# Performance work log

Hardware: AMD Instinct MI355X
Metric: run time of the kernel (lower is better)

Reference implementation:

```python
import jax, jax.numpy as jnp
import numpy as np

CH = 128
MID = CH // 4  # 32
B, H, W = 16, 128, 128


def _phi(x):
    # elu(x) + 1 (alpha=1)
    return jax.nn.elu(x) + 1.0


def setup_inputs() -> dict:
    key = jax.random.key(0)
    ks = jax.random.split(key, 6)
    x = jax.random.normal(ks[0], (B, CH, H, W), dtype=jnp.float32)
    Wq = jax.random.normal(ks[1], (MID, CH), dtype=jnp.float32) * 0.05
    Wk = jax.random.normal(ks[2], (MID, CH), dtype=jnp.float32) * 0.05
    Wv = jax.random.normal(ks[3], (MID, CH), dtype=jnp.float32) * 0.05
    Wout = jax.random.normal(ks[4], (CH, MID), dtype=jnp.float32) * 0.05
    gamma = jnp.ones((CH,), dtype=jnp.float32)
    beta = jnp.zeros((CH,), dtype=jnp.float32)
    return {"x": x, "Wq": Wq, "Wk": Wk, "Wv": Wv, "Wout": Wout,
            "gamma": gamma, "beta": beta}


def reference(x, Wq, Wk, Wv, Wout, gamma, beta):
    b, c, h, w = x.shape
    n = h * w
    xf = x.reshape(b, c, n)                      # [B, C, N]
    # 1x1 convs == channel matmuls
    Q = _phi(jnp.einsum('mc,bcn->bmn', Wq, xf))  # [B, M, N]
    K = _phi(jnp.einsum('mc,bcn->bmn', Wk, xf))  # [B, M, N]
    V = jnp.einsum('mc,bcn->bmn', Wv, xf)        # [B, M, N]
    # KV-first linear attention
    KV = jnp.einsum('bmn,bvn->bmv', K, V)        # [B, M, M]
    out = jnp.einsum('bmv,bvn->bmn', KV, Q) / (n + 1e-6)  # [B, M, N]
    Ks = jnp.sum(K, axis=-1, keepdims=True)      # [B, M, 1]
    denom = jnp.sum(Q * Ks, axis=1, keepdims=True) + 1e-6  # [B, 1, N]
    out = out / denom
    # output 1x1 conv
    y = jnp.einsum('cm,bmn->bcn', Wout, out).reshape(b, c, h, w)
    # BatchNorm2d (training-mode forward: batch statistics, biased var, eps=1e-5)
    mean = jnp.mean(y, axis=(0, 2, 3), keepdims=True)
    var = jnp.var(y, axis=(0, 2, 3), keepdims=True)
    y = (y - mean) * jax.lax.rsqrt(var + 1e-5)
    y = y * gamma[None, :, None, None] + beta[None, :, None, None]
    return y
```

## Files before the change

### kernel.cpp

```cpp
#include <hip/hip_runtime.h>

#define BB 16
#define CC 128
#define MM 32
#define NN 16384

#define WS_KV     0
#define WS_KS     16384
#define WS_SQ     16896
#define WS_QQ     17408
#define WS_YSUM   33792
#define WS_YSQ    33920
#define WS_ACCEND 34048
#define WS_W2     34304

typedef __bf16 bf16x8 __attribute__((ext_vector_type(8)));
typedef __bf16 bf16x4 __attribute__((ext_vector_type(4)));
typedef float  f32x16 __attribute__((ext_vector_type(16)));

union B8 { bf16x8 v8; bf16x4 v4[2]; };

__device__ __forceinline__ float phi_f(float z) {
    return z > 0.f ? z + 1.f : __expf(z);
}

__device__ __forceinline__ void lds_barrier() {
    asm volatile("s_waitcnt lgkmcnt(0)" ::: "memory");
    __builtin_amdgcn_sched_barrier(0);
    __builtin_amdgcn_s_barrier();
    __builtin_amdgcn_sched_barrier(0);
}

__global__ void zero_kernel(float* ws) {
    const int i = blockIdx.x * 256 + threadIdx.x;
    if (i < (WS_ACCEND / 4)) {
        float4 z; z.x = 0.f; z.y = 0.f; z.z = 0.f; z.w = 0.f;
        ((float4*)ws)[i] = z;
    }
}

__global__ __launch_bounds__(256) void projmfma_kernel(
    const float* __restrict__ x,
    const float* __restrict__ Wq, const float* __restrict__ Wk,
    const float* __restrict__ Wv,
    float* ws, float* __restrict__ qout)
{
    __shared__ __align__(16) char smem[71680];
    __bf16* Xh  = (__bf16*)smem;
    __bf16* ktH = (__bf16*)(smem + 34816);
    __bf16* ktL = (__bf16*)(smem + 44032);
    __bf16* vtH = (__bf16*)(smem + 53248);
    __bf16* vtL = (__bf16*)(smem + 62464);

    const int b = blockIdx.y;
    const int t = threadIdx.x;
    const int w = t >> 6;
    const int l = t & 63;
    const int g = l >> 5;
    const int ln31 = l & 31;

    bf16x8 wh[8], wl[8];
    if (w < 3) {
        const float* Wm = (w == 0) ? Wq : (w == 1) ? Wk : Wv;
        const float* wr = Wm + ln31 * CC;
        #pragma unroll
        for (int kt = 0; kt < 8; ++kt) {
            const int k0 = 16 * kt + 8 * g;
            #pragma unroll
            for (int j = 0; j < 8; ++j) {
                const float f = wr[k0 + j];
                const __bf16 h = (__bf16)f;
                wh[kt][j] = h;
                wl[kt][j] = (__bf16)(f - (float)h);
            }
        }
    }

    f32x16 kvA, ksA;
    bf16x8 ones;
    #pragma unroll
    for (int i = 0; i < 16; ++i) { kvA[i] = 0.f; ksA[i] = 0.f; }
    #pragma unroll
    for (int j = 0; j < 8; ++j) ones[j] = (__bf16)1.0f;

    const int px = t & 63;
    const int cb = t >> 6;

    const float* xbase = x + (size_t)b * CC * NN + (blockIdx.x << 9) + px;

    for (int tile = 0; tile < 8; ++tile) {
        const int cur = tile & 1;
        const int n0 = (blockIdx.x << 9) + (tile << 6);

        {
            const float* xp = xbase + (tile << 6);
            float xb[32];
            #pragma unroll
            for (int j = 0; j < 32; ++j)
                xb[j] = xp[(size_t)(cb * 32 + j) * NN];
            __bf16 hb[32];
            #pragma unroll
            for (int j = 0; j < 32; ++j) hb[j] = (__bf16)xb[j];
            #pragma unroll
            for (int q = 0; q < 4; ++q)
                *(bf16x8*)&Xh[cur * 8704 + px * 136 + cb * 32 + q * 8] =
                    *(bf16x8*)&hb[q * 8];
        }
        lds_barrier();

        if (w < 3) {
            f32x16 a0, a1;
            #pragma unroll
            for (int i = 0; i < 16; ++i) { a0[i] = 0.f; a1[i] = 0.f; }
            const __bf16* xh = Xh + cur * 8704;
            #pragma unroll
            for (int kt = 0; kt < 8; ++kt) {
                const int k0 = 16 * kt + 8 * g;
                const bf16x8 b0 = *(const bf16x8*)&xh[ln31 * 136 + k0];
                const bf16x8 b1 = *(const bf16x8*)&xh[(ln31 + 32) * 136 + k0];
                a0 = __builtin_amdgcn_mfma_f32_32x32x16_bf16(wh[kt], b0, a0, 0, 0, 0);
                a0 = __builtin_amdgcn_mfma_f32_32x32x16_bf16(wl[kt], b0, a0, 0, 0, 0);
                a1 = __builtin_amdgcn_mfma_f32_32x32x16_bf16(wh[kt], b1, a1, 0, 0, 0);
                a1 = __builtin_amdgcn_mfma_f32_32x32x16_bf16(wl[kt], b1, a1, 0, 0, 0);
            }
            if (w == 0) {
                float* qp = qout + (size_t)b * CC * NN + n0 + ln31;
                #pragma unroll
                for (int i = 0; i < 16; ++i) {
                    const int r = (i & 3) + 8 * (i >> 2) + 4 * g;
                    qp[(size_t)r * NN]      = phi_f(a0[i]);
                    qp[(size_t)r * NN + 32] = phi_f(a1[i]);
                }
            } else if (w == 1) {
                __bf16* kh = ktH + cur * 2304;
                __bf16* kl = ktL + cur * 2304;
                #pragma unroll
                for (int i = 0; i < 16; ++i) {
                    const int r = (i & 3) + 8 * (i >> 2) + 4 * g;
                    const float f0 = phi_f(a0[i]);
                    const float f1 = phi_f(a1[i]);
                    const __bf16 h0 = (__bf16)f0;
                    const __bf16 h1 = (__bf16)f1;
                    kh[r * 72 + ln31]      = h0;
                    kl[r * 72 + ln31]      = (__bf16)(f0 - (float)h0);
                    kh[r * 72 + 32 + ln31] = h1;
                    kl[r * 72 + 32 + ln31] = (__bf16)(f1 - (float)h1);
                }
            } else {
                __bf16* vh = vtH + cur * 2304;
                __bf16* vl = vtL + cur * 2304;
                #pragma unroll
                for (int i = 0; i < 16; ++i) {
                    const int r = (i & 3) + 8 * (i >> 2) + 4 * g;
                    const float f0 = a0[i];
                    const float f1 = a1[i];
                    const __bf16 h0 = (__bf16)f0;
                    const __bf16 h1 = (__bf16)f1;
                    vh[r * 72 + ln31]      = h0;
                    vl[r * 72 + ln31]      = (__bf16)(f0 - (float)h0);
                    vh[r * 72 + 32 + ln31] = h1;
                    vl[r * 72 + 32 + ln31] = (__bf16)(f1 - (float)h1);
                }
            }
        } else if (tile > 0) {
            const int pb = (cur ^ 1) * 2304;
            const __bf16* khp = ktH + pb + ln31 * 72;
            const __bf16* klp = ktL + pb + ln31 * 72;
            const __bf16* vhp = vtH + pb + ln31 * 72;
            const __bf16* vlp = vtL + pb + ln31 * 72;
            #pragma unroll
            for (int s = 0; s < 4; ++s) {
                const int k0 = s * 16 + g * 8;
                const bf16x8 akh = *(const bf16x8*)&khp[k0];
                const bf16x8 akl = *(const bf16x8*)&klp[k0];
                const bf16x8 bvh = *(const bf16x8*)&vhp[k0];
                const bf16x8 bvl = *(const bf16x8*)&vlp[k0];
                kvA = __builtin_amdgcn_mfma_f32_32x32x16_bf16(akh, bvh, kvA, 0, 0, 0);
                kvA = __builtin_amdgcn_mfma_f32_32x32x16_bf16(akh, bvl, kvA, 0, 0, 0);
                kvA = __builtin_amdgcn_mfma_f32_32x32x16_bf16(akl, bvh, kvA, 0, 0, 0);
                ksA = __builtin_amdgcn_mfma_f32_32x32x16_bf16(akh, ones, ksA, 0, 0, 0);
                ksA = __builtin_amdgcn_mfma_f32_32x32x16_bf16(akl, ones, ksA, 0, 0, 0);
            }
        }
        lds_barrier();
    }

    if (w == 3) {
        const int pb = 2304;
        const __bf16* khp = ktH + pb + ln31 * 72;
        const __bf16* klp = ktL + pb + ln31 * 72;
        const __bf16* vhp = vtH + pb + ln31 * 72;
        const __bf16* vlp = vtL + pb + ln31 * 72;
        #pragma unroll
        for (int s = 0; s < 4; ++s) {
            const int k0 = s * 16 + g * 8;
            const bf16x8 akh = *(const bf16x8*)&khp[k0];
            const bf16x8 akl = *(const bf16x8*)&klp[k0];
            const bf16x8 bvh = *(const bf16x8*)&vhp[k0];
            const bf16x8 bvl = *(const bf16x8*)&vlp[k0];
            kvA = __builtin_amdgcn_mfma_f32_32x32x16_bf16(akh, bvh, kvA, 0, 0, 0);
            kvA = __builtin_amdgcn_mfma_f32_32x32x16_bf16(akh, bvl, kvA, 0, 0, 0);
            kvA = __builtin_amdgcn_mfma_f32_32x32x16_bf16(akl, bvh, kvA, 0, 0, 0);
            ksA = __builtin_amdgcn_mfma_f32_32x32x16_bf16(akh, ones, ksA, 0, 0, 0);
            ksA = __builtin_amdgcn_mfma_f32_32x32x16_bf16(akl, ones, ksA, 0, 0, 0);
        }
        float* kvb = ws + WS_KV + (b << 10);
        #pragma unroll
        for (int i = 0; i < 16; ++i) {
            const int r = (i & 3) + 8 * (i >> 2) + 4 * g;
            atomicAdd(&kvb[r * 32 + ln31], kvA[i]);
        }
        if (ln31 == 0) {
            #pragma unroll
            for (int i = 0; i < 16; ++i) {
                const int r = (i & 3) + 8 * (i >> 2) + 4 * g;
                atomicAdd(&ws[WS_KS + (b << 5) + r], ksA[i]);
            }
        }
    }
}

__global__ __launch_bounds__(256) void qq_kernel(const float* qsrc, float* ws) {
    __shared__ __align__(16) char qsm[33792];
    __bf16* Qh = (__bf16*)qsm;
    __bf16* Ql = (__bf16*)(qsm + 16896);
    float*  red   = (float*)qsm;
    float*  sqred = (float*)(qsm + 17408);

    const int b = blockIdx.y;
    const int t = threadIdx.x;
    const int w = t >> 6;
    const int l = t & 63;
    const int g = l >> 5;
    const int ln31 = l & 31;

    const float* ksb = ws + WS_KS + (b << 5);
    const int n = (blockIdx.x << 8) + t;
    const float* qp = qsrc + (size_t)b * CC * NN + n;

    float qa[32];
    #pragma unroll
    for (int m = 0; m < 32; ++m) qa[m] = qp[(size_t)m * NN];

    float denom = 1e-6f;
    #pragma unroll
    for (int m = 0; m < 32; ++m) denom = fmaf(qa[m], ksb[m], denom);
    const float inv = 1.0f / (16384.0f * denom);
    #pragma unroll
    for (int m = 0; m < 32; ++m) qa[m] *= inv;

    #pragma unroll
    for (int m = 0; m < 32; ++m) {
        const __bf16 h = (__bf16)qa[m];
        Qh[m * 264 + t] = h;
        Ql[m * 264 + t] = (__bf16)(qa[m] - (float)h);
    }
    __syncthreads();

    f32x16 qqA, sqA;
    bf16x8 ones;
    #pragma unroll
    for (int i = 0; i < 16; ++i) { qqA[i] = 0.f; sqA[i] = 0.f; }
    #pragma unroll
    for (int j = 0; j < 8; ++j) ones[j] = (__bf16)1.0f;

    #pragma unroll
    for (int sub = 0; sub < 2; ++sub) {
        #pragma unroll
        for (int s = 0; s < 2; ++s) {
            const int k0 = (w << 6) + (sub << 5) + s * 16 + g * 8;
            const bf16x8 ah = *(const bf16x8*)&Qh[ln31 * 264 + k0];
            const bf16x8 al = *(const bf16x8*)&Ql[ln31 * 264 + k0];
            qqA = __builtin_amdgcn_mfma_f32_32x32x16_bf16(ah, ah, qqA, 0, 0, 0);
            qqA = __builtin_amdgcn_mfma_f32_32x32x16_bf16(ah, al, qqA, 0, 0, 0);
            qqA = __builtin_amdgcn_mfma_f32_32x32x16_bf16(al, ah, qqA, 0, 0, 0);
            sqA = __builtin_amdgcn_mfma_f32_32x32x16_bf16(ah, ones, sqA, 0, 0, 0);
            sqA = __builtin_amdgcn_mfma_f32_32x32x16_bf16(al, ones, sqA, 0, 0, 0);
        }
    }
    __syncthreads();

    #pragma unroll
    for (int i = 0; i < 16; ++i) red[t * 17 + i] = qqA[i];
    if (ln31 == 0) {
        #pragma unroll
        for (int i = 0; i < 16; ++i) {
            const int r = (i & 3) + 8 * (i >> 2) + 4 * g;
            sqred[(w << 5) + r] = sqA[i];
        }
    }
    __syncthreads();
    if (t < 64) {
        float* qqb = ws + WS_QQ + (b << 10);
        #pragma unroll
        for (int i = 0; i < 16; ++i) {
            const int r = (i & 3) + 8 * (i >> 2) + 4 * g;
            const float s = red[t*17+i] + red[(t+64)*17+i] + red[(t+128)*17+i] + red[(t+192)*17+i];
            atomicAdd(&qqb[r * 32 + ln31], s);
        }
    }
    if (t < 32) {
        const float s = sqred[t] + sqred[32 + t] + sqred[64 + t] + sqred[96 + t];
        atomicAdd(&ws[WS_SQ + (b << 5) + t], s);
    }
}

__global__ __launch_bounds__(128) void bnstat_kernel(const float* __restrict__ Wout,
                                                     float* ws) {
    const int b = blockIdx.x;
    const int c = threadIdx.x;
    const float* kvb = ws + WS_KV + (b << 10);
    const float* wo  = Wout + (c << 5);
    float w[32];
    #pragma unroll
    for (int v = 0; v < 32; ++v) w[v] = 0.f;
    for (int m = 0; m < 32; ++m) {
        const float wm = wo[m];
        #pragma unroll
        for (int v = 0; v < 32; ++v) w[v] = fmaf(wm, kvb[(m << 5) + v], w[v]);
    }
    float* w2b = ws + WS_W2 + (b << 12) + (c << 5);
    #pragma unroll
    for (int v = 0; v < 32; ++v) w2b[v] = w[v];

    const float* sq = ws + WS_SQ + (b << 5);
    const float* qq = ws + WS_QQ + (b << 10);
    float mb = 0.f;
    #pragma unroll
    for (int v = 0; v < 32; ++v) mb = fmaf(w[v], sq[v], mb);
    float qf = 0.f;
    for (int u = 0; u < 32; ++u) {
        float tacc = 0.f;
        #pragma unroll
        for (int v = 0; v < 32; ++v) tacc = fmaf(qq[(u << 5) + v], w[v], tacc);
        qf = fmaf(w[u], tacc, qf);
    }
    atomicAdd(&ws[WS_YSUM + c], mb);
    atomicAdd(&ws[WS_YSQ + c], qf);
}

__global__ __launch_bounds__(256) void out_kernel(const float* qsrc, const float* ws,
                                                  const float* __restrict__ gamma,
                                                  const float* __restrict__ beta,
                                                  float* out) {
    __shared__ __align__(16) __bf16 Qh[256 * 36];
    __shared__ __align__(16) __bf16 Ql[256 * 36];
    __shared__ float scs[CC];
    __shared__ float bis[CC];

    const int b = blockIdx.y;
    const int t = threadIdx.x;
    const int w = t >> 6;
    const int l = t & 63;
    const int g = l >> 5;
    const int ln31 = l & 31;

    if (t < CC) {
        const float invBN = 1.0f / 262144.0f;
        const float mean = ws[WS_YSUM + t] * invBN;
        const float var  = ws[WS_YSQ + t] * invBN - mean * mean;
        const float s = gamma[t] * rsqrtf(var + 1e-5f);
        scs[t] = s;
        bis[t] = fmaf(-mean, s, beta[t]);
    }

    const int n = (blockIdx.x << 8) + t;
    const float* ksb = ws + WS_KS + (b << 5);

    const float* qp = qsrc + (size_t)b * CC * NN + n;
    float qa[32];
    #pragma unroll
    for (int m = 0; m < 32; ++m) qa[m] = qp[(size_t)m * NN];

    float d0 = 1e-6f;
    #pragma unroll
    for (int m = 0; m < 32; ++m) d0 = fmaf(qa[m], ksb[m], d0);
    const float inv = 1.0f / (16384.0f * d0);
    #pragma unroll
    for (int m = 0; m < 32; ++m) qa[m] *= inv;

    {
        __bf16 qh[32], ql[32];
        #pragma unroll
        for (int m = 0; m < 32; ++m) {
            const __bf16 h = (__bf16)qa[m];
            qh[m] = h;
            ql[m] = (__bf16)(qa[m] - (float)h);
        }
        #pragma unroll
        for (int i = 0; i < 8; ++i) {
            *(bf16x4*)&Qh[t * 36 + i * 4] = *(bf16x4*)&qh[i * 4];
            *(bf16x4*)&Ql[t * 36 + i * 4] = *(bf16x4*)&ql[i * 4];
        }
    }
    __syncthreads();

    const float* w2b = ws + WS_W2 + (b << 12);
    float* ob = out + (size_t)b * CC * NN + (blockIdx.x << 8);

    #pragma unroll
    for (int cb = 0; cb < 4; ++cb) {
        bf16x8 ah[2], al[2];
        #pragma unroll
        for (int kt = 0; kt < 2; ++kt) {
            const float* wp = w2b + (cb * 32 + ln31) * 32 + kt * 16 + g * 8;
            #pragma unroll
            for (int j = 0; j < 8; ++j) {
                const float f = wp[j];
                const __bf16 h = (__bf16)f;
                ah[kt][j] = h;
                al[kt][j] = (__bf16)(f - (float)h);
            }
        }
        #pragma unroll
        for (int pg = 0; pg < 2; ++pg) {
            const int px0 = (w << 6) + (pg << 5);
            f32x16 acc;
            #pragma unroll
            for (int i = 0; i < 16; ++i) acc[i] = 0.f;
            #pragma unroll
            for (int kt = 0; kt < 2; ++kt) {
                const int k0 = kt * 16 + g * 8;
                const __bf16* qhp = &Qh[(px0 + ln31) * 36 + k0];
                const __bf16* qlp = &Ql[(px0 + ln31) * 36 + k0];
                B8 bh, bl;
                bh.v4[0] = *(const bf16x4*)&qhp[0];
                bh.v4[1] = *(const bf16x4*)&qhp[4];
                bl.v4[0] = *(const bf16x4*)&qlp[0];
                bl.v4[1] = *(const bf16x4*)&qlp[4];
                acc = __builtin_amdgcn_mfma_f32_32x32x16_bf16(ah[kt], bh.v8, acc, 0, 0, 0);
                acc = __builtin_amdgcn_mfma_f32_32x32x16_bf16(ah[kt], bl.v8, acc, 0, 0, 0);
                acc = __builtin_amdgcn_mfma_f32_32x32x16_bf16(al[kt], bh.v8, acc, 0, 0, 0);
            }
            #pragma unroll
            for (int i = 0; i < 16; ++i) {
                const int r = (i & 3) + 8 * (i >> 2) + 4 * g;
                const int c = cb * 32 + r;
                const float v = fmaf(scs[c], acc[i], bis[c]);
                __builtin_nontemporal_store(v, &ob[(size_t)c * NN + px0 + ln31]);
            }
        }
    }
}

extern "C" void kernel_launch(void* const* d_in, const int* in_sizes, int n_in,
                              void* d_out, int out_size, void* d_ws, size_t ws_size,
                              hipStream_t stream) {
    const float* x     = (const float*)d_in[0];
    const float* Wq    = (const float*)d_in[1];
    const float* Wk    = (const float*)d_in[2];
    const float* Wv    = (const float*)d_in[3];
    const float* Wout  = (const float*)d_in[4];
    const float* gamma = (const float*)d_in[5];
    const float* beta  = (const float*)d_in[6];
    float* ws  = (float*)d_ws;
    float* out = (float*)d_out;

    zero_kernel<<<34, 256, 0, stream>>>(ws);
    projmfma_kernel<<<dim3(32, 16), 256, 0, stream>>>(x, Wq, Wk, Wv, ws, out);
    qq_kernel<<<dim3(64, 16), 256, 0, stream>>>(out, ws);
    bnstat_kernel<<<16, 128, 0, stream>>>(Wout, ws);
    out_kernel<<<dim3(64, 16), 256, 0, stream>>>(out, ws, gamma, beta, out);
}
```

Baseline: 110.8 us.

## Split projection into one 64-pixel tile per block with prepacked bf16 weights

The projection kernel now handles one 64-pixel tile per block instead of looping over eight tiles, growing the grid from 512 to 4096 blocks. LDS is halved by dropping double buffering. A separate small kernel pre-splits the Q/K/V weights into hi/lo bf16 once, so each block loads packed weights instead of converting them. The KV accumulation is spread across all four waves and reduced in LDS before the global atomics. The aim is more occupancy and latency hiding. The cost is eight times more global atomics on KV/Ks, an extra kernel launch, and a weight reload per block.

```diff
diff --git a/kernel.cpp b/kernel.cpp
--- a/kernel.cpp
+++ b/kernel.cpp
@@ -13,6 +13,7 @@
 #define WS_YSQ    33920
 #define WS_ACCEND 34048
 #define WS_W2     34304
+#define WS_WPACK  99840
 
 typedef __bf16 bf16x8 __attribute__((ext_vector_type(8)));
 typedef __bf16 bf16x4 __attribute__((ext_vector_type(4)));
@@ -39,18 +40,33 @@
     }
 }
 
+__global__ void wpack_kernel(const float* __restrict__ Wq,
+                             const float* __restrict__ Wk,
+                             const float* __restrict__ Wv, float* ws) {
+    __bf16* wp = (__bf16*)(ws + WS_WPACK);
+    const int idx = blockIdx.x * 256 + threadIdx.x;
+    if (idx < 12288) {
+        const int mi  = idx >> 12;
+        const int rem = idx & 4095;
+        const float f = (mi == 0 ? Wq : mi == 1 ? Wk : Wv)[rem];
+        const __bf16 h = (__bf16)f;
+        wp[idx]         = h;
+        wp[12288 + idx] = (__bf16)(f - (float)h);
+    }
+}
+
 __global__ __launch_bounds__(256) void projmfma_kernel(
-    const float* __restrict__ x,
-    const float* __restrict__ Wq, const float* __restrict__ Wk,
-    const float* __restrict__ Wv,
+    const float* __restrict__ x, const float* ws_c,
     float* ws, float* __restrict__ qout)
 {
-    __shared__ __align__(16) char smem[71680];
+    __shared__ __align__(16) char smem[35840];
     __bf16* Xh  = (__bf16*)smem;
-    __bf16* ktH = (__bf16*)(smem + 34816);
-    __bf16* ktL = (__bf16*)(smem + 44032);
-    __bf16* vtH = (__bf16*)(smem + 53248);
-    __bf16* vtL = (__bf16*)(smem + 62464);
+    __bf16* ktH = (__bf16*)(smem + 17408);
+    __bf16* ktL = (__bf16*)(smem + 22016);
+    __bf16* vtH = (__bf16*)(smem + 26624);
+    __bf16* vtL = (__bf16*)(smem + 31232);
+    float*  red   = (float*)smem;
+    float*  ksred = (float*)(smem + 17408);
 
     const int b = blockIdx.y;
     const int t = threadIdx.x;
@@ -59,22 +75,86 @@
     const int g = l >> 5;
     const int ln31 = l & 31;
 
+    const int n0 = blockIdx.x << 6;
+
     bf16x8 wh[8], wl[8];
     if (w < 3) {
-        const float* Wm = (w == 0) ? Wq : (w == 1) ? Wk : Wv;
-        const float* wr = Wm + ln31 * CC;
+        const __bf16* wp = (const __bf16*)(ws_c + WS_WPACK) + w * 4096 + ln31 * 128;
+        #pragma unroll
+        for (int kt = 0; kt < 8; ++kt) {
+            wh[kt] = *(const bf16x8*)&wp[16 * kt + 8 * g];
+            wl[kt] = *(const bf16x8*)&wp[12288 + 16 * kt + 8 * g];
+        }
+    }
+
+    {
+        const int px = t & 63;
+        const int cb = t >> 6;
+        const float* xp = x + (size_t)b * CC * NN + n0 + px;
+        float xb[32];
+        #pragma unroll
+        for (int j = 0; j < 32; ++j)
+            xb[j] = xp[(size_t)(cb * 32 + j) * NN];
+        __bf16 hb[32];
+        #pragma unroll
+        for (int j = 0; j < 32; ++j) hb[j] = (__bf16)xb[j];
+        #pragma unroll
+        for (int q = 0; q < 4; ++q)
+            *(bf16x8*)&Xh[px * 136 + cb * 32 + q * 8] = *(bf16x8*)&hb[q * 8];
+    }
+    lds_barrier();
+
+    if (w < 3) {
+        f32x16 a0, a1;
+        #pragma unroll
+        for (int i = 0; i < 16; ++i) { a0[i] = 0.f; a1[i] = 0.f; }
         #pragma unroll
         for (int kt = 0; kt < 8; ++kt) {
             const int k0 = 16 * kt + 8 * g;
-            #pragma unroll
-            for (int j = 0; j < 8; ++j) {
-                const float f = wr[k0 + j];
-                const __bf16 h = (__bf16)f;
-                wh[kt][j] = h;
-                wl[kt][j] = (__bf16)(f - (float)h);
-            }
-        }
-    }
+            const bf16x8 b0 = *(const bf16x8*)&Xh[ln31 * 136 + k0];
+            const bf16x8 b1 = *(const bf16x8*)&Xh[(ln31 + 32) * 136 + k0];
+            a0 = __builtin_amdgcn_mfma_f32_32x32x16_bf16(wh[kt], b0, a0, 0, 0, 0);
+            a0 = __builtin_amdgcn_mfma_f32_32x32x16_bf16(wl[kt], b0, a0, 0, 0, 0);
+            a1 = __builtin_amdgcn_mfma_f32_32x32x16_bf16(wh[kt], b1, a1, 0, 0, 0);
+            a1 = __builtin_amdgcn_mfma_f32_32x32x16_bf16(wl[kt], b1, a1, 0, 0, 0);
+        }
+        if (w == 0) {
+            float* qp = qout + (size_t)b * CC * NN + n0 + ln31;
+            #pragma unroll
+            for (int i = 0; i < 16; ++i) {
+                const int r = (i & 3) + 8 * (i >> 2) + 4 * g;
+                qp[(size_t)r * NN]      = phi_f(a0[i]);
+                qp[(size_t)r * NN + 32] = phi_f(a1[i]);
+            }
+        } else if (w == 1) {
+            #pragma unroll
+            for (int i = 0; i < 16; ++i) {
+                const int r = (i & 3) + 8 * (i >> 2) + 4 * g;
+                const float f0 = phi_f(a0[i]);
+                const float f1 = phi_f(a1[i]);
+                const __bf16 h0 = (__bf16)f0;
+                const __bf16 h1 = (__bf16)f1;
+                ktH[r * 72 + ln31]      = h0;
+                ktL[r * 72 + ln31]      = (__bf16)(f0 - (float)h0);
+                ktH[r * 72 + 32 + ln31] = h1;
+                ktL[r * 72 + 32 + ln31] = (__bf16)(f1 - (float)h1);
+            }
+        } else {
+            #pragma unroll
+            for (int i = 0; i < 16; ++i) {
+                const int r = (i & 3) + 8 * (i >> 2) + 4 * g;
+                const float f0 = a0[i];
+                const float f1 = a1[i];
+                const __bf16 h0 = (__bf16)f0;
+                const __bf16 h1 = (__bf16)f1;
+                vtH[r * 72 + ln31]      = h0;
+                vtL[r * 72 + ln31]      = (__bf16)(f0 - (float)h0);
+                vtH[r * 72 + 32 + ln31] = h1;
+                vtL[r * 72 + 32 + ln31] = (__bf16)(f1 - (float)h1);
+            }
+        }
+    }
+    lds_barrier();
 
     f32x16 kvA, ksA;
     bf16x8 ones;
@@ -82,141 +162,42 @@
     for (int i = 0; i < 16; ++i) { kvA[i] = 0.f; ksA[i] = 0.f; }
     #pragma unroll
     for (int j = 0; j < 8; ++j) ones[j] = (__bf16)1.0f;
-
-    const int px = t & 63;
-    const int cb = t >> 6;
-
-    const float* xbase = x + (size_t)b * CC * NN + (blockIdx.x << 9) + px;
-
-    for (int tile = 0; tile < 8; ++tile) {
-        const int cur = tile & 1;
-        const int n0 = (blockIdx.x << 9) + (tile << 6);
-
-        {
-            const float* xp = xbase + (tile << 6);
-            float xb[32];
-            #pragma unroll
-            for (int j = 0; j < 32; ++j)
-                xb[j] = xp[(size_t)(cb * 32 + j) * NN];
-            __bf16 hb[32];
-            #pragma unroll
-            for (int j = 0; j < 32; ++j) hb[j] = (__bf16)xb[j];
-            #pragma unroll
-            for (int q = 0; q < 4; ++q)
-                *(bf16x8*)&Xh[cur * 8704 + px * 136 + cb * 32 + q * 8] =
-                    *(bf16x8*)&hb[q * 8];
-        }
-        lds_barrier();
-
-        if (w < 3) {
-            f32x16 a0, a1;
-            #pragma unroll
-            for (int i = 0; i < 16; ++i) { a0[i] = 0.f; a1[i] = 0.f; }
-            const __bf16* xh = Xh + cur * 8704;
-            #pragma unroll
-            for (int kt = 0; kt < 8; ++kt) {
-                const int k0 = 16 * kt + 8 * g;
-                const bf16x8 b0 = *(const bf16x8*)&xh[ln31 * 136 + k0];
-                const bf16x8 b1 = *(const bf16x8*)&xh[(ln31 + 32) * 136 + k0];
-                a0 = __builtin_amdgcn_mfma_f32_32x32x16_bf16(wh[kt], b0, a0, 0, 0, 0);
-                a0 = __builtin_amdgcn_mfma_f32_32x32x16_bf16(wl[kt], b0, a0, 0, 0, 0);
-                a1 = __builtin_amdgcn_mfma_f32_32x32x16_bf16(wh[kt], b1, a1, 0, 0, 0);
-                a1 = __builtin_amdgcn_mfma_f32_32x32x16_bf16(wl[kt], b1, a1, 0, 0, 0);
-            }
-            if (w == 0) {
-                float* qp = qout + (size_t)b * CC * NN + n0 + ln31;
-                #pragma unroll
-                for (int i = 0; i < 16; ++i) {
-                    const int r = (i & 3) + 8 * (i >> 2) + 4 * g;
-                    qp[(size_t)r * NN]      = phi_f(a0[i]);
-                    qp[(size_t)r * NN + 32] = phi_f(a1[i]);
-                }
-            } else if (w == 1) {
-                __bf16* kh = ktH + cur * 2304;
-                __bf16* kl = ktL + cur * 2304;
-                #pragma unroll
-                for (int i = 0; i < 16; ++i) {
-                    const int r = (i & 3) + 8 * (i >> 2) + 4 * g;
-                    const float f0 = phi_f(a0[i]);
-                    const float f1 = phi_f(a1[i]);
-                    const __bf16 h0 = (__bf16)f0;
-                    const __bf16 h1 = (__bf16)f1;
-                    kh[r * 72 + ln31]      = h0;
-                    kl[r * 72 + ln31]      = (__bf16)(f0 - (float)h0);
-                    kh[r * 72 + 32 + ln31] = h1;
-                    kl[r * 72 + 32 + ln31] = (__bf16)(f1 - (float)h1);
-                }
-            } else {
-                __bf16* vh = vtH + cur * 2304;
-                __bf16* vl = vtL + cur * 2304;
-                #pragma unroll
-                for (int i = 0; i < 16; ++i) {
-                    const int r = (i & 3) + 8 * (i >> 2) + 4 * g;
-                    const float f0 = a0[i];
-                    const float f1 = a1[i];
-                    const __bf16 h0 = (__bf16)f0;
-                    const __bf16 h1 = (__bf16)f1;
-                    vh[r * 72 + ln31]      = h0;
-                    vl[r * 72 + ln31]      = (__bf16)(f0 - (float)h0);
-                    vh[r * 72 + 32 + ln31] = h1;
-                    vl[r * 72 + 32 + ln31] = (__bf16)(f1 - (float)h1);
-                }
-            }
-        } else if (tile > 0) {
-            const int pb = (cur ^ 1) * 2304;
-            const __bf16* khp = ktH + pb + ln31 * 72;
-            const __bf16* klp = ktL + pb + ln31 * 72;
-            const __bf16* vhp = vtH + pb + ln31 * 72;
-            const __bf16* vlp = vtL + pb + ln31 * 72;
-            #pragma unroll
-            for (int s = 0; s < 4; ++s) {
-                const int k0 = s * 16 + g * 8;
-                const bf16x8 akh = *(const bf16x8*)&khp[k0];
-                const bf16x8 akl = *(const bf16x8*)&klp[k0];
-                const bf16x8 bvh = *(const bf16x8*)&vhp[k0];
-                const bf16x8 bvl = *(const bf16x8*)&vlp[k0];
-                kvA = __builtin_amdgcn_mfma_f32_32x32x16_bf16(akh, bvh, kvA, 0, 0, 0);
-                kvA = __builtin_amdgcn_mfma_f32_32x32x16_bf16(akh, bvl, kvA, 0, 0, 0);
-                kvA = __builtin_amdgcn_mfma_f32_32x32x16_bf16(akl, bvh, kvA, 0, 0, 0);
-                ksA = __builtin_amdgcn_mfma_f32_32x32x16_bf16(akh, ones, ksA, 0, 0, 0);
-                ksA = __builtin_amdgcn_mfma_f32_32x32x16_bf16(akl, ones, ksA, 0, 0, 0);
-            }
-        }
-        lds_barrier();
-    }
-
-    if (w == 3) {
-        const int pb = 2304;
-        const __bf16* khp = ktH + pb + ln31 * 72;
-        const __bf16* klp = ktL + pb + ln31 * 72;
-        const __bf16* vhp = vtH + pb + ln31 * 72;
-        const __bf16* vlp = vtL + pb + ln31 * 72;
-        #pragma unroll
-        for (int s = 0; s < 4; ++s) {
-            const int k0 = s * 16 + g * 8;
-            const bf16x8 akh = *(const bf16x8*)&khp[k0];
-            const bf16x8 akl = *(const bf16x8*)&klp[k0];
-            const bf16x8 bvh = *(const bf16x8*)&vhp[k0];
-            const bf16x8 bvl = *(const bf16x8*)&vlp[k0];
-            kvA = __builtin_amdgcn_mfma_f32_32x32x16_bf16(akh, bvh, kvA, 0, 0, 0);
-            kvA = __builtin_amdgcn_mfma_f32_32x32x16_bf16(akh, bvl, kvA, 0, 0, 0);
-            kvA = __builtin_amdgcn_mfma_f32_32x32x16_bf16(akl, bvh, kvA, 0, 0, 0);
-            ksA = __builtin_amdgcn_mfma_f32_32x32x16_bf16(akh, ones, ksA, 0, 0, 0);
-            ksA = __builtin_amdgcn_mfma_f32_32x32x16_bf16(akl, ones, ksA, 0, 0, 0);
-        }
-        float* kvb = ws + WS_KV + (b << 10);
+    {
+        const int k0 = 16 * w + 8 * g;
+        const bf16x8 akh = *(const bf16x8*)&ktH[ln31 * 72 + k0];
+        const bf16x8 akl = *(const bf16x8*)&ktL[ln31 * 72 + k0];
+        const bf16x8 bvh = *(const bf16x8*)&vtH[ln31 * 72 + k0];
+        const bf16x8 bvl = *(const bf16x8*)&vtL[ln31 * 72 + k0];
+        kvA = __builtin_amdgcn_mfma_f32_32x32x16_bf16(akh, bvh, kvA, 0, 0, 0);
+        kvA = __builtin_amdgcn_mfma_f32_32x32x16_bf16(akh, bvl, kvA, 0, 0, 0);
+        kvA = __builtin_amdgcn_mfma_f32_32x32x16_bf16(akl, bvh, kvA, 0, 0, 0);
+        ksA = __builtin_amdgcn_mfma_f32_32x32x16_bf16(akh, ones, ksA, 0, 0, 0);
+        ksA = __builtin_amdgcn_mfma_f32_32x32x16_bf16(akl, ones, ksA, 0, 0, 0);
+    }
+    lds_barrier();
+
+    #pragma unroll
+    for (int i = 0; i < 16; ++i) red[t * 17 + i] = kvA[i];
+    if (ln31 == 0) {
         #pragma unroll
         for (int i = 0; i < 16; ++i) {
             const int r = (i & 3) + 8 * (i >> 2) + 4 * g;
-            atomicAdd(&kvb[r * 32 + ln31], kvA[i]);
-        }
-        if (ln31 == 0) {
-            #pragma unroll
-            for (int i = 0; i < 16; ++i) {
-                const int r = (i & 3) + 8 * (i >> 2) + 4 * g;
-                atomicAdd(&ws[WS_KS + (b << 5) + r], ksA[i]);
-            }
-        }
+            ksred[(w << 5) + r] = ksA[i];
+        }
+    }
+    lds_barrier();
+    if (t < 64) {
+        float* kvb = ws + WS_KV + (b << 10);
+        #pragma unroll
+        for (int i = 0; i < 16; ++i) {
+            const int r = (i & 3) + 8 * (i >> 2) + 4 * g;
+            const float s = red[t*17+i] + red[(t+64)*17+i] + red[(t+128)*17+i] + red[(t+192)*17+i];
+            atomicAdd(&kvb[r * 32 + ln31], s);
+        }
+    }
+    if (t < 32) {
+        const float s = ksred[t] + ksred[32 + t] + ksred[64 + t] + ksred[96 + t];
+        atomicAdd(&ws[WS_KS + (b << 5) + t], s);
     }
 }
 
@@ -457,7 +438,8 @@
     float* out = (float*)d_out;
 
     zero_kernel<<<34, 256, 0, stream>>>(ws);
-    projmfma_kernel<<<dim3(32, 16), 256, 0, stream>>>(x, Wq, Wk, Wv, ws, out);
+    wpack_kernel<<<48, 256, 0, stream>>>(Wq, Wk, Wv, ws);
+    projmfma_kernel<<<dim3(256, 16), 256, 0, stream>>>(x, ws, ws, out);
     qq_kernel<<<dim3(64, 16), 256, 0, stream>>>(out, ws);
     bnstat_kernel<<<16, 128, 0, stream>>>(Wout, ws);
     out_kernel<<<dim3(64, 16), 256, 0, stream>>>(out, ws, gamma, beta, out);
```

After: 132.5 us. 1.2x slower.
